# Optimization experiments

Hardware: AMD Instinct MI355X
Metric: run time of the kernel (lower is better)

## Reference

```python
import jax, jax.numpy as jnp
import numpy as np

N = 100000      # nodes
E = 1600000     # edges
G = 64          # graphs in batch
F_IN = 128
HID = 16        # per-head hidden of conv1
H = 8           # heads of conv1
F_OUT = 16
NEG_SLOPE = 0.2


def setup_inputs() -> dict:
    key = jax.random.key(0)
    ks = jax.random.split(key, 11)
    x = jax.random.normal(ks[0], (N, F_IN), jnp.float32)
    edge_index = jax.random.randint(ks[1], (2, E), 0, N, jnp.int32)
    batch = jnp.sort(jax.random.randint(ks[2], (N,), 0, G, jnp.int32))
    s_in = 1.0 / np.sqrt(F_IN)
    s_h = 1.0 / np.sqrt(HID)
    s_mid = 1.0 / np.sqrt(H * HID)
    W1 = jax.random.normal(ks[3], (F_IN, H * HID), jnp.float32) * s_in
    att1_src = jax.random.normal(ks[4], (H, HID), jnp.float32) * s_h
    att1_dst = jax.random.normal(ks[5], (H, HID), jnp.float32) * s_h
    b1 = jnp.zeros((H * HID,), jnp.float32)
    W2 = jax.random.normal(ks[6], (H * HID, F_OUT), jnp.float32) * s_mid
    att2_src = jax.random.normal(ks[7], (1, F_OUT), jnp.float32) * (1.0 / np.sqrt(F_OUT))
    att2_dst = jax.random.normal(ks[8], (1, F_OUT), jnp.float32) * (1.0 / np.sqrt(F_OUT))
    b2 = jnp.zeros((F_OUT,), jnp.float32)
    return {"x": x, "edge_index": edge_index, "batch": batch,
            "W1": W1, "att1_src": att1_src, "att1_dst": att1_dst, "b1": b1,
            "W2": W2, "att2_src": att2_src, "att2_dst": att2_dst, "b2": b2}


def _gat_conv(x, edge_index, W, a_src, a_dst, b, concat):
    """PyG GATConv: h = xW; e_ij = leaky_relu(a_src.h_j + a_dst.h_i);
    softmax over in-edges of each dst node i; out_i = sum_j alpha_ij h_j."""
    src, dst = edge_index[0], edge_index[1]
    n = x.shape[0]
    nh, c = a_src.shape
    h = (x @ W).reshape(n, nh, c)                      # [N,H,C]
    a_s = jnp.einsum('nhc,hc->nh', h, a_src)           # [N,H]
    a_d = jnp.einsum('nhc,hc->nh', h, a_dst)
    e = jax.nn.leaky_relu(a_s[src] + a_d[dst], NEG_SLOPE)   # [E,H]
    m = jax.lax.stop_gradient(jax.ops.segment_max(e, dst, num_segments=n))
    ex = jnp.exp(e - m[dst])
    denom = jax.ops.segment_sum(ex, dst, num_segments=n)
    alpha = ex / (denom[dst] + 1e-16)                  # [E,H]
    msg = h[src] * alpha[:, :, None]                   # [E,H,C]
    out = jax.ops.segment_sum(msg, dst, num_segments=n)  # [N,H,C]
    out = out.reshape(n, nh * c) if concat else out.mean(axis=1)
    return out + b


def reference(x, edge_index, batch, W1, att1_src, att1_dst, b1,
              W2, att2_src, att2_dst, b2):
    h = _gat_conv(x, edge_index, W1, att1_src, att1_dst, b1, concat=True)
    h = jax.nn.elu(h)
    # F.dropout(p=0.6, training=False) -> identity in eval mode
    h = _gat_conv(h, edge_index, W2, att2_src, att2_dst, b2, concat=False)
    counts = jax.ops.segment_sum(jnp.ones((h.shape[0],), h.dtype), batch, num_segments=G)
    pooled = jax.ops.segment_sum(h, batch, num_segments=G) / jnp.maximum(counts, 1.0)[:, None]
    return jax.nn.log_softmax(pooled, axis=1)
```

## Files before the change

kernel.cpp:

```cpp
#include <hip/hip_runtime.h>
#include <cstdint>
#include <cstddef>

typedef unsigned short ushort_t;
typedef unsigned int uint_t;
typedef __attribute__((ext_vector_type(8))) short bf16x8;
typedef __attribute__((ext_vector_type(4))) float f32x4;

#define NBMAX 1024
#define EPB   16384
#define LDK   136

__device__ inline ushort_t f2bf(float f) {
  uint_t u = __float_as_uint(f);
  uint_t r = (u + 0x7fffu + ((u >> 16) & 1u)) >> 16;
  return (ushort_t)r;
}
__device__ inline float bfl(uint_t u) { return __uint_as_float(u << 16); }
__device__ inline float bfh(uint_t u) { return __uint_as_float(u & 0xffff0000u); }
__device__ inline float bf1(ushort_t v) { return __uint_as_float(((uint_t)v) << 16); }


__global__ void bucket_hist_kernel(const int* __restrict__ edst, int* __restrict__ gcount,
                                   int* __restrict__ myBase, int E, int NB) {
  __shared__ int hist[NBMAX];
  int t = threadIdx.x;
  int blk = blockIdx.x;
  for (int i = t; i < NB; i += 256) hist[i] = 0;
  __syncthreads();
  int b0 = blk * EPB, e1 = min(b0 + EPB, E);
  for (int i = b0 + t; i < e1; i += 256) atomicAdd(&hist[edst[i] >> 7], 1);
  __syncthreads();
  for (int i = t; i < NB; i += 256) {
    int c = hist[i];
    myBase[(size_t)blk * NB + i] = c ? atomicAdd(&gcount[i], c) : 0;
  }
}

__global__ void bucket_scan_kernel(const int* __restrict__ gcount, int* __restrict__ boff, int NB) {
  __shared__ int ws[16];
  int t = threadIdx.x;
  int lane = t & 63, w = t >> 6;
  int v = (t < NB) ? gcount[t] : 0;
  for (int o = 1; o < 64; o <<= 1) { int y = __shfl_up(v, o); if (lane >= o) v += y; }
  if (lane == 63) ws[w] = v;
  __syncthreads();
  if (t < 16) {
    int s = ws[t];
    for (int o = 1; o < 16; o <<= 1) { int y = __shfl_up(s, o); if (t >= o) s += y; }
    ws[t] = s;
  }
  __syncthreads();
  if (w > 0) v += ws[w - 1];
  if (t < NB) boff[t + 1] = v;
  if (t == 0) boff[0] = 0;
}

__global__ void bucket_scatter_kernel(const int* __restrict__ esrc, const int* __restrict__ edst,
                                      const int* __restrict__ boff, const int* __restrict__ myBase,
                                      uint_t* __restrict__ pairs, int E, int NB) {
  __shared__ int cursor[NBMAX];
  int t = threadIdx.x;
  int blk = blockIdx.x;
  for (int i = t; i < NB; i += 256) cursor[i] = boff[i] + myBase[(size_t)blk * NB + i];
  __syncthreads();
  int b0 = blk * EPB, e1 = min(b0 + EPB, E);
  for (int i = b0 + t; i < e1; i += 256) {
    int d = edst[i], s = esrc[i];
    int pos = atomicAdd(&cursor[d >> 7], 1);
    pairs[pos] = ((uint_t)(d & 127) << 25) | (uint_t)s;
  }
}

__global__ void bucket_csr_kernel(const uint_t* __restrict__ pairs, const int* __restrict__ boff,
                                  int* __restrict__ rowptr, int* __restrict__ csr, int n, int NB) {
  __shared__ int cnt[128];
  __shared__ int ws2[2];
  int b = blockIdx.x;
  int t = threadIdx.x;
  int lo = boff[b], hi = boff[b + 1];
  int D0 = b << 7;
  cnt[t] = 0;
  __syncthreads();
  for (int i = lo + t; i < hi; i += 128) atomicAdd(&cnt[pairs[i] >> 25], 1);
  __syncthreads();
  int lane = t & 63, w = t >> 6;
  int v = cnt[t];
  int vx = v;
  for (int o = 1; o < 64; o <<= 1) { int y = __shfl_up(vx, o); if (lane >= o) vx += y; }
  if (lane == 63) ws2[w] = vx;
  __syncthreads();
  int incl = vx + (w ? ws2[0] : 0);
  int excl = incl - v;
  int d = D0 + t;
  if (d <= n) rowptr[d] = lo + excl;
  __syncthreads();
  cnt[t] = excl;
  __syncthreads();
  for (int i = lo + t; i < hi; i += 128) {
    uint_t pr = pairs[i];
    int pos = atomicAdd(&cnt[pr >> 25], 1);
    csr[lo + pos] = (int)(pr & 0x1FFFFFFu);
  }
}

__global__ void gemm1_att1_kernel(const float* __restrict__ x, const float* __restrict__ W,
                                  const float* __restrict__ asw, const float* __restrict__ adw,
                                  ushort_t* __restrict__ h1b, float* __restrict__ a_s,
                                  float* __restrict__ a_d, int n) {
  __shared__ ushort_t wT[128 * LDK];
  int t = threadIdx.x;
  {
    int nn = t & 127;
    int kp0 = t >> 7;
    for (int kp = kp0; kp < 64; kp += 2) {
      float w0 = W[(size_t)(2 * kp) * 128 + nn];
      float w1 = W[(size_t)(2 * kp + 1) * 128 + nn];
      *(uint_t*)&wT[nn * LDK + 2 * kp] = (uint_t)f2bf(w0) | ((uint_t)f2bf(w1) << 16);
    }
  }
  __syncthreads();

  int lane = t & 63, w = t >> 6;
  int g = lane >> 4, cl = lane & 15;

  #pragma unroll
  for (int rt = 0; rt < 2; ++rt) {
    int rowA = blockIdx.x * 128 + rt * 64 + w * 16 + cl;
    const float* xr = x + (size_t)(rowA < n ? rowA : 0) * 128;

    bf16x8 afr[4];
    #pragma unroll
    for (int c = 0; c < 4; ++c) {
      float4 v0 = *(const float4*)(xr + c * 32 + g * 8);
      float4 v1 = *(const float4*)(xr + c * 32 + g * 8 + 4);
      bf16x8 a;
      a[0] = (short)f2bf(v0.x); a[1] = (short)f2bf(v0.y);
      a[2] = (short)f2bf(v0.z); a[3] = (short)f2bf(v0.w);
      a[4] = (short)f2bf(v1.x); a[5] = (short)f2bf(v1.y);
      a[6] = (short)f2bf(v1.z); a[7] = (short)f2bf(v1.w);
      afr[c] = a;
    }

    int orow0 = blockIdx.x * 128 + rt * 64 + w * 16 + g * 4;
    #pragma unroll 2
    for (int tt = 0; tt < 8; ++tt) {
      f32x4 acc = {0.f, 0.f, 0.f, 0.f};
      #pragma unroll
      for (int c = 0; c < 4; ++c) {
        bf16x8 bfr = *(const bf16x8*)&wT[(tt * 16 + cl) * LDK + c * 32 + g * 8];
        acc = __builtin_amdgcn_mfma_f32_16x16x32_bf16(afr[c], bfr, acc, 0, 0, 0);
      }
      float asv = asw[tt * 16 + cl], adv = adw[tt * 16 + cl];
      float ps[4], pd[4];
      ushort_t hb[4];
      #pragma unroll
      for (int r = 0; r < 4; ++r) {
        float v = acc[r];
        hb[r] = f2bf(v);
        ps[r] = v * asv; pd[r] = v * adv;
      }
      #pragma unroll
      for (int o = 1; o < 16; o <<= 1) {
        #pragma unroll
        for (int r = 0; r < 4; ++r) { ps[r] += __shfl_xor(ps[r], o); pd[r] += __shfl_xor(pd[r], o); }
      }
      #pragma unroll
      for (int r = 0; r < 4; ++r) {
        int rr = orow0 + r;
        if (rr < n) {
          h1b[(size_t)rr * 128 + tt * 16 + cl] = hb[r];
          if (cl == 0) {
            a_s[(size_t)rr * 8 + tt] = ps[r];
            a_d[(size_t)rr * 8 + tt] = pd[r];
          }
        }
      }
    }
  }
}

__global__ void alpha1_kernel(const int* __restrict__ rowptr, const int* __restrict__ csr_src,
                              const float* __restrict__ a_s, const float* __restrict__ a_d,
                              ushort_t* __restrict__ alpha1, int n) {
  __shared__ float e_lds[4][64][8];
  int t = threadIdx.x & 63;
  int w = threadIdx.x >> 6;
  int dst = blockIdx.x * 4 + w;
  if (dst >= n) return;
  int beg = rowptr[dst], end = rowptr[dst + 1];
  int deg = end - beg;
  if (deg == 0) return;
  int h = t & 7, el = t >> 3;
  float adv = a_d[(size_t)dst * 8 + h];
  float M = -1e30f, S = 0.f;

  if (deg <= 64) {
    int nch = (deg + 7) >> 3;
    for (int it = 0; it < nch; ++it) {
      int eidx = beg + it * 8 + el;
      bool valid = eidx < end;
      int s = csr_src[valid ? eidx : beg];
      float eraw = a_s[(size_t)s * 8 + h] + adv;
      eraw = eraw > 0.f ? eraw : 0.2f * eraw;
      e_lds[w][it * 8 + el][h] = eraw;
      float e = valid ? eraw : -1e30f;
      float m = e;
      m = fmaxf(m, __shfl_xor(m, 8));
      m = fmaxf(m, __shfl_xor(m, 16));
      m = fmaxf(m, __shfl_xor(m, 32));
      float nm = fmaxf(M, m);
      float p = valid ? __expf(e - nm) : 0.f;
      float ps = p;
      ps += __shfl_xor(ps, 8);
      ps += __shfl_xor(ps, 16);
      ps += __shfl_xor(ps, 32);
      S = S * __expf(M - nm) + ps;
      M = nm;
    }
    float inv = 1.f / (S + 1e-16f);
    for (int it = 0; it < nch; ++it) {
      int eidx = beg + it * 8 + el;
      if (eidx < end) {
        float e = e_lds[w][it * 8 + el][h];
        alpha1[(size_t)eidx * 8 + h] = f2bf(__expf(e - M) * inv);
      }
    }
  } else {
    for (int base = beg; base < end; base += 8) {
      int eidx = base + el;
      bool valid = eidx < end;
      int s = csr_src[valid ? eidx : beg];
      float e = a_s[(size_t)s * 8 + h] + adv;
      e = e > 0.f ? e : 0.2f * e;
      e = valid ? e : -1e30f;
      float m = e;
      m = fmaxf(m, __shfl_xor(m, 8));
      m = fmaxf(m, __shfl_xor(m, 16));
      m = fmaxf(m, __shfl_xor(m, 32));
      float nm = fmaxf(M, m);
      float p = valid ? __expf(e - nm) : 0.f;
      float ps = p;
      ps += __shfl_xor(ps, 8);
      ps += __shfl_xor(ps, 16);
      ps += __shfl_xor(ps, 32);
      S = S * __expf(M - nm) + ps;
      M = nm;
    }
    float inv = 1.f / (S + 1e-16f);
    for (int base = beg; base < end; base += 8) {
      int eidx = base + el;
      if (eidx < end) {
        int s = csr_src[eidx];
        float e = a_s[(size_t)s * 8 + h] + adv;
        e = e > 0.f ? e : 0.2f * e;
        alpha1[(size_t)eidx * 8 + h] = f2bf(__expf(e - M) * inv);
      }
    }
  }
}

__global__ void gat1_agg_kernel(const int* __restrict__ rowptr, const int* __restrict__ csr_src,
                                const ushort_t* __restrict__ h1b,
                                const ushort_t* __restrict__ alpha1,
                                const float* __restrict__ b1, ushort_t* __restrict__ hmidb, int n) {
  int lane = threadIdx.x & 63;
  int w = threadIdx.x >> 6;
  int dst = blockIdx.x * 4 + w;
  if (dst >= n) return;
  int beg = rowptr[dst], end = rowptr[dst + 1];
  int slot = lane >> 4, c8 = lane & 15;
  int hh = c8 >> 1;
  float acc[8] = {};
  #pragma unroll 2
  for (int e = beg + slot; e < end; e += 4) {
    int si = csr_src[e];
    float a = bf1(alpha1[(size_t)e * 8 + hh]);
    uint4 hv = *(const uint4*)(h1b + (size_t)si * 128 + c8 * 8);
    acc[0] = fmaf(a, bfl(hv.x), acc[0]);
    acc[1] = fmaf(a, bfh(hv.x), acc[1]);
    acc[2] = fmaf(a, bfl(hv.y), acc[2]);
    acc[3] = fmaf(a, bfh(hv.y), acc[3]);
    acc[4] = fmaf(a, bfl(hv.z), acc[4]);
    acc[5] = fmaf(a, bfh(hv.z), acc[5]);
    acc[6] = fmaf(a, bfl(hv.w), acc[6]);
    acc[7] = fmaf(a, bfh(hv.w), acc[7]);
  }
  #pragma unroll
  for (int i = 0; i < 8; ++i) {
    acc[i] += __shfl_xor(acc[i], 16);
    acc[i] += __shfl_xor(acc[i], 32);
  }
  if (slot == 0) {
    ushort_t ob[8];
    #pragma unroll
    for (int i = 0; i < 8; ++i) {
      float v = acc[i] + b1[c8 * 8 + i];
      v = v > 0.f ? v : (__expf(v) - 1.f);
      ob[i] = f2bf(v);
    }
    *(uint4*)(hmidb + (size_t)dst * 128 + c8 * 8) = *(uint4*)ob;
  }
}

__global__ void gemm2_att2_kernel(const ushort_t* __restrict__ hmidb, const float* __restrict__ W2,
                                  const float* __restrict__ asw, const float* __restrict__ adw,
                                  ushort_t* __restrict__ h2b, float* __restrict__ a_s2,
                                  float* __restrict__ a_d2, int n) {
  __shared__ ushort_t wT[16 * LDK];
  int t = threadIdx.x;
  if (t < 128) {
    int nn = t & 15, kp0 = t >> 4;
    for (int kp = kp0; kp < 64; kp += 8) {
      float w0 = W2[(size_t)(2 * kp) * 16 + nn];
      float w1 = W2[(size_t)(2 * kp + 1) * 16 + nn];
      *(uint_t*)&wT[nn * LDK + 2 * kp] = (uint_t)f2bf(w0) | ((uint_t)f2bf(w1) << 16);
    }
  }
  __syncthreads();

  int lane = t & 63, w = t >> 6;
  int g = lane >> 4, cl = lane & 15;
  int rowA = blockIdx.x * 64 + w * 16 + cl;
  const ushort_t* hr = hmidb + (size_t)(rowA < n ? rowA : 0) * 128;

  f32x4 acc = {0.f, 0.f, 0.f, 0.f};
  #pragma unroll
  for (int c = 0; c < 4; ++c) {
    bf16x8 afr = *(const bf16x8*)(hr + c * 32 + g * 8);
    bf16x8 bfr = *(const bf16x8*)&wT[cl * LDK + c * 32 + g * 8];
    acc = __builtin_amdgcn_mfma_f32_16x16x32_bf16(afr, bfr, acc, 0, 0, 0);
  }
  float asv = asw[cl], adv = adw[cl];
  float ps[4], pd[4];
  ushort_t hb[4];
  #pragma unroll
  for (int r = 0; r < 4; ++r) {
    float v = acc[r];
    hb[r] = f2bf(v);
    ps[r] = v * asv; pd[r] = v * adv;
  }
  #pragma unroll
  for (int o = 1; o < 16; o <<= 1) {
    #pragma unroll
    for (int r = 0; r < 4; ++r) { ps[r] += __shfl_xor(ps[r], o); pd[r] += __shfl_xor(pd[r], o); }
  }
  int orow0 = blockIdx.x * 64 + w * 16 + g * 4;
  #pragma unroll
  for (int r = 0; r < 4; ++r) {
    int rr = orow0 + r;
    if (rr < n) {
      h2b[(size_t)rr * 16 + cl] = hb[r];
      if (cl == 0) { a_s2[rr] = ps[r]; a_d2[rr] = pd[r]; }
    }
  }
}

__global__ void alpha2_kernel(const int* __restrict__ rowptr, const int* __restrict__ csr_src,
                              const float* __restrict__ a_s2, const float* __restrict__ a_d2,
                              float* __restrict__ alpha2, int n) {
  int t = threadIdx.x & 63;
  int w = threadIdx.x >> 6;
  int dst = blockIdx.x * 4 + w;
  if (dst >= n) return;
  int beg = rowptr[dst], end = rowptr[dst + 1];
  int deg = end - beg;
  if (deg == 0) return;
  float adv = a_d2[dst];

  if (deg <= 64) {
    int eidx = beg + t;
    bool valid = eidx < end;
    int s = csr_src[valid ? eidx : beg];
    float e = a_s2[s] + adv;
    e = e > 0.f ? e : 0.2f * e;
    float ev = valid ? e : -1e30f;
    float m = ev;
    #pragma unroll
    for (int o = 1; o < 64; o <<= 1) m = fmaxf(m, __shfl_xor(m, o));
    float p = valid ? __expf(ev - m) : 0.f;
    float S = p;
    #pragma unroll
    for (int o = 1; o < 64; o <<= 1) S += __shfl_xor(S, o);
    if (valid) alpha2[eidx] = p / (S + 1e-16f);
    return;
  }

  float M = -1e30f, S = 0.f;
  for (int base = beg; base < end; base += 64) {
    int eidx = base + t;
    bool valid = eidx < end;
    int s = csr_src[valid ? eidx : beg];
    float e = a_s2[s] + adv;
    e = e > 0.f ? e : 0.2f * e;
    e = valid ? e : -1e30f;
    float m = e;
    #pragma unroll
    for (int o = 1; o < 64; o <<= 1) m = fmaxf(m, __shfl_xor(m, o));
    float nm = fmaxf(M, m);
    float p = valid ? __expf(e - nm) : 0.f;
    float ps = p;
    #pragma unroll
    for (int o = 1; o < 64; o <<= 1) ps += __shfl_xor(ps, o);
    S = S * __expf(M - nm) + ps;
    M = nm;
  }
  float inv = 1.f / (S + 1e-16f);
  for (int base = beg; base < end; base += 64) {
    int eidx = base + t;
    if (eidx < end) {
      int s = csr_src[eidx];
      float e = a_s2[s] + adv;
      e = e > 0.f ? e : 0.2f * e;
      alpha2[eidx] = __expf(e - M) * inv;
    }
  }
}

__global__ void gat2_agg_kernel(const int* __restrict__ rowptr, const int* __restrict__ csr_src,
                                const ushort_t* __restrict__ h2b,
                                const float* __restrict__ alpha2, const float* __restrict__ b2,
                                const int* __restrict__ batch,
                                float* __restrict__ pooled, float* __restrict__ cntb,
                                int n, int G) {
  __shared__ float pooledL[17][16];
  __shared__ float cntL[17];
  __shared__ int   s_lds[16][16];
  __shared__ float a_lds[16][16];
  int t = threadIdx.x;
  if (t < 17) cntL[t] = 0.f;
  for (int i = t; i < 17 * 16; i += 256) ((float*)pooledL)[i] = 0.f;
  __syncthreads();

  int grp = t >> 4, c = t & 15;
  int dst = blockIdx.x * 16 + grp;
  int gfirst = batch[blockIdx.x * 16];

  if (dst < n) {
    int beg = rowptr[dst], end = rowptr[dst + 1];
    float acc = 0.f;
    for (int base = beg; base < end; base += 16) {
      int idx = base + c;
      bool v = idx < end;
      s_lds[grp][c] = v ? csr_src[idx] : 0;
      a_lds[grp][c] = v ? alpha2[idx] : 0.f;
      #pragma unroll
      for (int j = 0; j < 16; ++j) {
        acc = fmaf(a_lds[grp][j], bf1(h2b[(size_t)s_lds[grp][j] * 16 + c]), acc);
      }
    }
    float v = acc + b2[c];
    int g = batch[dst];
    int gi = g - gfirst;
    if (gi <= 16) {
      atomicAdd(&pooledL[gi][c], v);
      if (c == 0) atomicAdd(&cntL[gi], 1.f);
    } else {
      atomicAdd(&pooled[g * 16 + c], v);
      if (c == 0) atomicAdd(&cntb[g], 1.f);
    }
  }
  __syncthreads();

  int w = t >> 5, lane32 = t & 31;
  for (int gi = w; gi < 17; gi += 8) {
    if (cntL[gi] > 0.f) {
      int g = gfirst + gi;
      if (lane32 < 16) atomicAdd(&pooled[g * 16 + lane32], pooledL[gi][lane32]);
      else if (lane32 == 16) atomicAdd(&cntb[g], cntL[gi]);
    }
  }
}

__global__ void final_kernel(const float* __restrict__ pooled, const float* __restrict__ cntb,
                             float* __restrict__ out, int G) {
  int g = threadIdx.x;
  if (g >= G) return;
  float c = fmaxf(cntb[g], 1.f);
  float v[16];
  float m = -1e30f;
  #pragma unroll
  for (int i = 0; i < 16; ++i) { v[i] = pooled[g * 16 + i] / c; m = fmaxf(m, v[i]); }
  float s = 0.f;
  #pragma unroll
  for (int i = 0; i < 16; ++i) s += __expf(v[i] - m);
  float ls = logf(s);
  #pragma unroll
  for (int i = 0; i < 16; ++i) out[g * 16 + i] = v[i] - m - ls;
}

extern "C" void kernel_launch(void* const* d_in, const int* in_sizes, int n_in,
                              void* d_out, int out_size, void* d_ws, size_t ws_size,
                              hipStream_t stream) {
  const float* x    = (const float*)d_in[0];
  const int*   eidx = (const int*)  d_in[1];
  const int*   batch= (const int*)  d_in[2];
  const float* W1   = (const float*)d_in[3];
  const float* as1w = (const float*)d_in[4];
  const float* ad1w = (const float*)d_in[5];
  const float* b1   = (const float*)d_in[6];
  const float* W2   = (const float*)d_in[7];
  const float* as2w = (const float*)d_in[8];
  const float* ad2w = (const float*)d_in[9];
  const float* b2   = (const float*)d_in[10];
  float* out = (float*)d_out;

  int N = in_sizes[0] / 128;
  int E = in_sizes[1] / 2;
  int G = out_size / 16;
  const int* esrc = eidx;
  const int* edst = eidx + E;

  int NB = (N + 127) >> 7;
  int nblkA = (E + EPB - 1) / EPB;

  char* p = (char*)d_ws;
  auto alloc = [&](size_t bytes) {
    char* r = p;
    p += (bytes + 255) & ~(size_t)255;
    return r;
  };
  ushort_t* h1b = (ushort_t*)alloc((size_t)N * 128 * 2);
  ushort_t* hmidb = (ushort_t*)alloc((size_t)N * 128 * 2);
  ushort_t* h2b = (ushort_t*)alloc((size_t)N * 16 * 2);
  float* as1  = (float*)alloc((size_t)N * 8 * 4);
  float* ad1  = (float*)alloc((size_t)N * 8 * 4);
  float* as2  = (float*)alloc((size_t)N * 4);
  float* ad2  = (float*)alloc((size_t)N * 4);
  size_t a1sz = (size_t)E * 8 * 2, a2sz = (size_t)E * 4;
  size_t unionSz = a1sz + a2sz;
  char* U = alloc(unionSz);
  uint_t* pairs = (uint_t*)U;
  ushort_t* alpha1 = (ushort_t*)U;
  float* alpha2 = (float*)(U + a1sz);
  float* pooled = (float*)alloc((size_t)(G * 16 + G) * 4);
  float* cntb = pooled + G * 16;
  int* rowptr = (int*)alloc((size_t)(N + 1) * 4);
  int* csr    = (int*)alloc((size_t)E * 4);
  int* gcount = (int*)alloc((size_t)(NBMAX + 1) * 4);
  int* boff   = (int*)alloc((size_t)(NBMAX + 1) * 4);
  int* myBase = (int*)alloc((size_t)nblkA * NB * 4);

  hipMemsetAsync(gcount, 0, (size_t)(NBMAX + 1) * 4, stream);
  hipMemsetAsync(pooled, 0, (size_t)(G * 16 + G) * 4, stream);

  bucket_hist_kernel<<<nblkA, 256, 0, stream>>>(edst, gcount, myBase, E, NB);
  bucket_scan_kernel<<<1, 1024, 0, stream>>>(gcount, boff, NB);
  bucket_scatter_kernel<<<nblkA, 256, 0, stream>>>(esrc, edst, boff, myBase, pairs, E, NB);
  bucket_csr_kernel<<<NB, 128, 0, stream>>>(pairs, boff, rowptr, csr, N, NB);

  gemm1_att1_kernel<<<(N + 127) / 128, 256, 0, stream>>>(x, W1, as1w, ad1w, h1b, as1, ad1, N);
  alpha1_kernel<<<(N + 3) / 4, 256, 0, stream>>>(rowptr, csr, as1, ad1, alpha1, N);
  gat1_agg_kernel<<<(N + 3) / 4, 256, 0, stream>>>(rowptr, csr, h1b, alpha1, b1, hmidb, N);
  gemm2_att2_kernel<<<(N + 63) / 64, 256, 0, stream>>>(hmidb, W2, as2w, ad2w, h2b, as2, ad2, N);
  alpha2_kernel<<<(N + 3) / 4, 256, 0, stream>>>(rowptr, csr, as2, ad2, alpha2, N);
  gat2_agg_kernel<<<(N + 15) / 16, 256, 0, stream>>>(rowptr, csr, h2b, alpha2, b2, batch, pooled, cntb, N, G);
  final_kernel<<<1, (G + 63) / 64 * 64, 0, stream>>>(pooled, cntb, out, G);
}
```

Measured before the change: 404.3 us.

## Fuse layer-1 attention softmax with aggregation and fold pooled memset into scan

Merges the alpha1 and gat1 aggregation kernels into one kernel. Normalized attention weights now stay in LDS (or are recomputed for high-degree nodes) instead of making a bf16 round trip through global memory, which removes one launch and the per-edge alpha1 traffic. The pooled-buffer memset moves into the bucket scan kernel, and the edges-per-block for bucketing drops from 16384 to 4096 to give more blocks. The trade-off is that the fused kernel may use more registers and LDS, and high-degree nodes do the score computation twice.

Measured after the change: 383.0 us. 1.06x faster.

```diff
diff --git a/kernel.cpp b/kernel.cpp
--- a/kernel.cpp
+++ b/kernel.cpp
@@ -8,7 +8,7 @@
 typedef __attribute__((ext_vector_type(4))) float f32x4;
 
 #define NBMAX 1024
-#define EPB   16384
+#define EPB   4096
 #define LDK   136
 
 __device__ inline ushort_t f2bf(float f) {
@@ -37,9 +37,11 @@
   }
 }
 
-__global__ void bucket_scan_kernel(const int* __restrict__ gcount, int* __restrict__ boff, int NB) {
+__global__ void bucket_scan_kernel(const int* __restrict__ gcount, int* __restrict__ boff, int NB,
+                                   float* __restrict__ pooled, int poolsz) {
   __shared__ int ws[16];
   int t = threadIdx.x;
+  for (int i = t; i < poolsz; i += 1024) pooled[i] = 0.f;
   int lane = t & 63, w = t >> 6;
   int v = (t < NB) ? gcount[t] : 0;
   for (int o = 1; o < 64; o <<= 1) { int y = __shfl_up(v, o); if (lane >= o) v += y; }
@@ -180,9 +182,10 @@
   }
 }
 
-__global__ void alpha1_kernel(const int* __restrict__ rowptr, const int* __restrict__ csr_src,
-                              const float* __restrict__ a_s, const float* __restrict__ a_d,
-                              ushort_t* __restrict__ alpha1, int n) {
+__global__ void gat1_fused_kernel(const int* __restrict__ rowptr, const int* __restrict__ csr_src,
+                                  const ushort_t* __restrict__ h1b,
+                                  const float* __restrict__ a_s, const float* __restrict__ a_d,
+                                  const float* __restrict__ b1, ushort_t* __restrict__ hmidb, int n) {
   __shared__ float e_lds[4][64][8];
   int t = threadIdx.x & 63;
   int w = threadIdx.x >> 6;
@@ -190,12 +193,16 @@
   if (dst >= n) return;
   int beg = rowptr[dst], end = rowptr[dst + 1];
   int deg = end - beg;
-  if (deg == 0) return;
+
   int h = t & 7, el = t >> 3;
   float adv = a_d[(size_t)dst * 8 + h];
   float M = -1e30f, S = 0.f;
 
-  if (deg <= 64) {
+  int slot = t >> 4, c8 = t & 15;
+  int hh = c8 >> 1;
+  float acc[8] = {};
+
+  if (deg > 0 && deg <= 64) {
     int nch = (deg + 7) >> 3;
     for (int it = 0; it < nch; ++it) {
       int eidx = beg + it * 8 + el;
@@ -220,13 +227,24 @@
     }
     float inv = 1.f / (S + 1e-16f);
     for (int it = 0; it < nch; ++it) {
-      int eidx = beg + it * 8 + el;
-      if (eidx < end) {
-        float e = e_lds[w][it * 8 + el][h];
-        alpha1[(size_t)eidx * 8 + h] = f2bf(__expf(e - M) * inv);
-      }
-    }
-  } else {
+      int pos = it * 8 + el;
+      if (beg + pos < end)
+        e_lds[w][pos][h] = __expf(e_lds[w][pos][h] - M) * inv;
+    }
+    for (int i = slot; i < deg; i += 4) {
+      int si = csr_src[beg + i];
+      float a = e_lds[w][i][hh];
+      uint4 hv = *(const uint4*)(h1b + (size_t)si * 128 + c8 * 8);
+      acc[0] = fmaf(a, bfl(hv.x), acc[0]);
+      acc[1] = fmaf(a, bfh(hv.x), acc[1]);
+      acc[2] = fmaf(a, bfl(hv.y), acc[2]);
+      acc[3] = fmaf(a, bfh(hv.y), acc[3]);
+      acc[4] = fmaf(a, bfl(hv.z), acc[4]);
+      acc[5] = fmaf(a, bfh(hv.z), acc[5]);
+      acc[6] = fmaf(a, bfl(hv.w), acc[6]);
+      acc[7] = fmaf(a, bfh(hv.w), acc[7]);
+    }
+  } else if (deg > 64) {
     for (int base = beg; base < end; base += 8) {
       int eidx = base + el;
       bool valid = eidx < end;
@@ -248,44 +266,26 @@
       M = nm;
     }
     float inv = 1.f / (S + 1e-16f);
-    for (int base = beg; base < end; base += 8) {
-      int eidx = base + el;
-      if (eidx < end) {
-        int s = csr_src[eidx];
-        float e = a_s[(size_t)s * 8 + h] + adv;
-        e = e > 0.f ? e : 0.2f * e;
-        alpha1[(size_t)eidx * 8 + h] = f2bf(__expf(e - M) * inv);
-      }
-    }
-  }
-}
-
-__global__ void gat1_agg_kernel(const int* __restrict__ rowptr, const int* __restrict__ csr_src,
-                                const ushort_t* __restrict__ h1b,
-                                const ushort_t* __restrict__ alpha1,
-                                const float* __restrict__ b1, ushort_t* __restrict__ hmidb, int n) {
-  int lane = threadIdx.x & 63;
-  int w = threadIdx.x >> 6;
-  int dst = blockIdx.x * 4 + w;
-  if (dst >= n) return;
-  int beg = rowptr[dst], end = rowptr[dst + 1];
-  int slot = lane >> 4, c8 = lane & 15;
-  int hh = c8 >> 1;
-  float acc[8] = {};
-  #pragma unroll 2
-  for (int e = beg + slot; e < end; e += 4) {
-    int si = csr_src[e];
-    float a = bf1(alpha1[(size_t)e * 8 + hh]);
-    uint4 hv = *(const uint4*)(h1b + (size_t)si * 128 + c8 * 8);
-    acc[0] = fmaf(a, bfl(hv.x), acc[0]);
-    acc[1] = fmaf(a, bfh(hv.x), acc[1]);
-    acc[2] = fmaf(a, bfl(hv.y), acc[2]);
-    acc[3] = fmaf(a, bfh(hv.y), acc[3]);
-    acc[4] = fmaf(a, bfl(hv.z), acc[4]);
-    acc[5] = fmaf(a, bfh(hv.z), acc[5]);
-    acc[6] = fmaf(a, bfl(hv.w), acc[6]);
-    acc[7] = fmaf(a, bfh(hv.w), acc[7]);
-  }
+    float Mh = __shfl(M, hh);
+    float invh = __shfl(inv, hh);
+    float advh = __shfl(adv, hh);
+    for (int i = slot; i < deg; i += 4) {
+      int si = csr_src[beg + i];
+      float eraw = a_s[(size_t)si * 8 + hh] + advh;
+      eraw = eraw > 0.f ? eraw : 0.2f * eraw;
+      float a = __expf(eraw - Mh) * invh;
+      uint4 hv = *(const uint4*)(h1b + (size_t)si * 128 + c8 * 8);
+      acc[0] = fmaf(a, bfl(hv.x), acc[0]);
+      acc[1] = fmaf(a, bfh(hv.x), acc[1]);
+      acc[2] = fmaf(a, bfl(hv.y), acc[2]);
+      acc[3] = fmaf(a, bfh(hv.y), acc[3]);
+      acc[4] = fmaf(a, bfl(hv.z), acc[4]);
+      acc[5] = fmaf(a, bfh(hv.z), acc[5]);
+      acc[6] = fmaf(a, bfl(hv.w), acc[6]);
+      acc[7] = fmaf(a, bfh(hv.w), acc[7]);
+    }
+  }
+
   #pragma unroll
   for (int i = 0; i < 8; ++i) {
     acc[i] += __shfl_xor(acc[i], 16);
@@ -527,12 +527,9 @@
   float* ad1  = (float*)alloc((size_t)N * 8 * 4);
   float* as2  = (float*)alloc((size_t)N * 4);
   float* ad2  = (float*)alloc((size_t)N * 4);
-  size_t a1sz = (size_t)E * 8 * 2, a2sz = (size_t)E * 4;
-  size_t unionSz = a1sz + a2sz;
-  char* U = alloc(unionSz);
+  char* U = alloc((size_t)E * 4);
   uint_t* pairs = (uint_t*)U;
-  ushort_t* alpha1 = (ushort_t*)U;
-  float* alpha2 = (float*)(U + a1sz);
+  float* alpha2 = (float*)U;
   float* pooled = (float*)alloc((size_t)(G * 16 + G) * 4);
   float* cntb = pooled + G * 16;
   int* rowptr = (int*)alloc((size_t)(N + 1) * 4);
@@ -542,16 +539,14 @@
   int* myBase = (int*)alloc((size_t)nblkA * NB * 4);
 
   hipMemsetAsync(gcount, 0, (size_t)(NBMAX + 1) * 4, stream);
-  hipMemsetAsync(pooled, 0, (size_t)(G * 16 + G) * 4, stream);
 
   bucket_hist_kernel<<<nblkA, 256, 0, stream>>>(edst, gcount, myBase, E, NB);
-  bucket_scan_kernel<<<1, 1024, 0, stream>>>(gcount, boff, NB);
+  bucket_scan_kernel<<<1, 1024, 0, stream>>>(gcount, boff, NB, pooled, G * 16 + G);
   bucket_scatter_kernel<<<nblkA, 256, 0, stream>>>(esrc, edst, boff, myBase, pairs, E, NB);
   bucket_csr_kernel<<<NB, 128, 0, stream>>>(pairs, boff, rowptr, csr, N, NB);
 
   gemm1_att1_kernel<<<(N + 127) / 128, 256, 0, stream>>>(x, W1, as1w, ad1w, h1b, as1, ad1, N);
-  alpha1_kernel<<<(N + 3) / 4, 256, 0, stream>>>(rowptr, csr, as1, ad1, alpha1, N);
-  gat1_agg_kernel<<<(N + 3) / 4, 256, 0, stream>>>(rowptr, csr, h1b, alpha1, b1, hmidb, N);
+  gat1_fused_kernel<<<(N + 3) / 4, 256, 0, stream>>>(rowptr, csr, h1b, as1, ad1, b1, hmidb, N);
   gemm2_att2_kernel<<<(N + 63) / 64, 256, 0, stream>>>(hmidb, W2, as2w, ad2w, h2b, as2, ad2, N);
   alpha2_kernel<<<(N + 3) / 4, 256, 0, stream>>>(rowptr, csr, as2, ad2, alpha2, N);
   gat2_agg_kernel<<<(N + 15) / 16, 256, 0, stream>>>(rowptr, csr, h2b, alpha2, b2, batch, pooled, cntb, N, G);
```
